# Optimization experiments

Hardware: AMD Instinct MI355X
Metric: run time of the kernel (lower is better)

## Reference

```python
import jax, jax.numpy as jnp
import numpy as np

B, S, D = 2, 2048, 768
H = 12
DH = D // H
EPS = 1e-12


def setup_inputs() -> dict:
    key = jax.random.key(0)
    ks = jax.random.split(key, 16)
    s = 0.02
    return {
        "hidden_states": jax.random.normal(ks[0], (B, S, D), jnp.float32),
        "attention_mask": jnp.zeros((B, 1, 1, S), jnp.float32),
        "position_bias": jax.random.normal(ks[1], (1, H, S, S), jnp.float32),
        "q_w": jax.random.normal(ks[2], (D, D), jnp.float32) * s,
        "q_b": jnp.zeros((D,), jnp.float32),
        "k_w": jax.random.normal(ks[3], (D, D), jnp.float32) * s,
        "k_b": jnp.zeros((D,), jnp.float32),
        "v_w": jax.random.normal(ks[4], (D, D), jnp.float32) * s,
        "v_b": jnp.zeros((D,), jnp.float32),
        "o_w": jax.random.normal(ks[5], (D, D), jnp.float32) * s,
        "o_b": jnp.zeros((D,), jnp.float32),
        "ln_w": jnp.ones((D,), jnp.float32),
        "ln_b": jnp.zeros((D,), jnp.float32),
    }


def _split_heads(x):
    # [B, S, D] -> [B, H, S, DH]
    b, s, _ = x.shape
    return x.reshape(b, s, H, DH).transpose(0, 2, 1, 3)


def reference(hidden_states, attention_mask, position_bias,
              q_w, q_b, k_w, k_b, v_w, v_b, o_w, o_b, ln_w, ln_b):
    # nn.Linear: y = x @ W.T + b (W stored [out, in])
    q = _split_heads(hidden_states @ q_w.T + q_b)
    k = _split_heads(hidden_states @ k_w.T + k_b)
    v = _split_heads(hidden_states @ v_w.T + v_b)

    scale = 1.0 / jnp.sqrt(jnp.asarray(DH, hidden_states.dtype))
    scores = jnp.einsum('bhqd,bhkd->bhqk', q, k) * scale
    scores = scores + position_bias + attention_mask
    probs = jax.nn.softmax(scores, axis=-1)

    c = jnp.einsum('bhqk,bhkd->bhqd', probs, v)
    c = c.transpose(0, 2, 1, 3).reshape(hidden_states.shape[0], -1, D)
    o = c @ o_w.T + o_b

    # residual + LayerNorm (dropout is identity at eval)
    x = o + hidden_states
    mu = jnp.mean(x, axis=-1, keepdims=True)
    var = jnp.mean(jnp.square(x - mu), axis=-1, keepdims=True)
    out = (x - mu) * jax.lax.rsqrt(var + EPS) * ln_w + ln_b
    return out
```

## Files before the change

### kernel.cpp

```cpp
#include <hip/hip_runtime.h>
#include <math.h>

typedef unsigned short u16;
typedef float f32x4 __attribute__((ext_vector_type(4)));
typedef __bf16 bf16x8 __attribute__((ext_vector_type(8)));

#define B_ 2
#define S_ 2048
#define D_ 768
#define H_ 12
#define DH_ 64

__device__ __forceinline__ u16 f2bf(float x) {
  union { float f; unsigned u; } v; v.f = x;
  unsigned r = v.u + 0x7fffu + ((v.u >> 16) & 1u);
  return (u16)(r >> 16);
}

__device__ __forceinline__ f32x4 zero4() { f32x4 z = {0.f, 0.f, 0.f, 0.f}; return z; }

__device__ __forceinline__ f32x4 mfma16(bf16x8 a, bf16x8 b, f32x4 c) {
  return __builtin_amdgcn_mfma_f32_16x16x32_bf16(a, b, c, 0, 0, 0);
}

__device__ __forceinline__ void gload_lds16(const void* g, void* l) {
  __builtin_amdgcn_global_load_lds((const __attribute__((address_space(1))) void*)g,
                                   (__attribute__((address_space(3))) void*)l, 16, 0, 0);
}

__global__ void cvt_kernel(const float* __restrict__ hid, const float* __restrict__ qw,
                           const float* __restrict__ kw, const float* __restrict__ vw,
                           const float* __restrict__ ow, u16* __restrict__ Hb,
                           u16* __restrict__ Wb) {
  const int NH = B_ * S_ * D_;
  const int NW = D_ * D_;
  const int T4 = (NH + 4 * NW) >> 2;
  int stride = gridDim.x * blockDim.x;
  for (int i = blockIdx.x * blockDim.x + threadIdx.x; i < T4; i += stride) {
    int e = i << 2;
    const float* src; u16* dst;
    if (e < NH) { src = hid + e; dst = Hb + e; }
    else {
      int o = e - NH;
      int m = o / NW, oo = o - m * NW;
      src = (m == 0 ? qw : m == 1 ? kw : m == 2 ? vw : ow) + oo;
      dst = Wb + o;
    }
    f32x4 v = *(const f32x4*)src;
    uint2 o2;
    o2.x = (unsigned)f2bf(v[0]) | ((unsigned)f2bf(v[1]) << 16);
    o2.y = (unsigned)f2bf(v[2]) | ((unsigned)f2bf(v[3]) << 16);
    *(uint2*)dst = o2;
  }
}

#define BM 128
#define BN 128
#define BK 64

__global__ __launch_bounds__(256) void gemm_kernel(
    const u16* __restrict__ A, const u16* __restrict__ W,
    const float* __restrict__ bq, const float* __restrict__ bk, const float* __restrict__ bv,
    u16* __restrict__ Qb, u16* __restrict__ Kb, u16* __restrict__ Vtmp,
    float* __restrict__ Of, const float* __restrict__ bO, int mode)
{
  __shared__ __align__(16) u16 As[BM * BK];
  __shared__ __align__(16) u16 Bs[BN * BK];
  int t = threadIdx.x;
  int lane = t & 63, w = t >> 6;
  int wr = w >> 1, wc = w & 1;
  int l15 = lane & 15, l4 = lane >> 4;
  int m0 = blockIdx.y * BM, n0 = blockIdx.x * BN;

  f32x4 acc[4][4];
#pragma unroll
  for (int i = 0; i < 4; ++i)
#pragma unroll
    for (int j = 0; j < 4; ++j) acc[i][j] = zero4();

  const int K = D_;
  for (int k0 = 0; k0 < K; k0 += BK) {
    __syncthreads();
#pragma unroll
    for (int p = 0; p < 4; ++p) {
      int seg = p * 4 + w;
      int bd = seg * 64 + lane;
      int row = bd >> 3;
      int slot = (bd & 7) ^ (row & 7);
      gload_lds16(A + (size_t)(m0 + row) * K + k0 + slot * 8, (char*)As + seg * 1024);
      gload_lds16(W + (size_t)(n0 + row) * K + k0 + slot * 8, (char*)Bs + seg * 1024);
    }
    __syncthreads();
#pragma unroll
    for (int kk = 0; kk < 2; ++kk) {
      bf16x8 af[4], bfr[4];
#pragma unroll
      for (int i = 0; i < 4; ++i) {
        int ra = wr * 64 + i * 16 + l15;
        af[i] = *(const bf16x8*)((const char*)As + ra * 128 +
                                 ((kk * 64 + (l4 << 4)) ^ ((ra & 7) << 4)));
        int rb = wc * 64 + i * 16 + l15;
        bfr[i] = *(const bf16x8*)((const char*)Bs + rb * 128 +
                                  ((kk * 64 + (l4 << 4)) ^ ((rb & 7) << 4)));
      }
#pragma unroll
      for (int i = 0; i < 4; ++i)
#pragma unroll
        for (int j = 0; j < 4; ++j)
          acc[i][j] = mfma16(af[i], bfr[j], acc[i][j]);
    }
  }

  if (mode == 0) {
    int mat = n0 / D_;
    int ncol0 = (n0 - mat * D_) + wc * 64;
    const float* bias = (mat == 0) ? bq : (mat == 1 ? bk : bv);
    u16* outp = (mat == 0) ? Qb : (mat == 1 ? Kb : Vtmp);
    float scale = (mat == 0) ? 0.125f : 1.0f;
    int h = ncol0 >> 6;
#pragma unroll
    for (int j = 0; j < 4; ++j) {
      int d = j * 16 + l15;
      float bvv = bias[ncol0 + d];
#pragma unroll
      for (int i = 0; i < 4; ++i) {
#pragma unroll
        for (int r = 0; r < 4; ++r) {
          int m = m0 + wr * 64 + i * 16 + (l4 << 2) + r;
          int bb = m >> 11, ss = m & 2047;
          float val = (acc[i][j][r] + bvv) * scale;
          outp[(((size_t)bb * H_ + h) * S_ + ss) * DH_ + d] = f2bf(val);
        }
      }
    }
  } else {
#pragma unroll
    for (int j = 0; j < 4; ++j) {
      int n = n0 + wc * 64 + j * 16 + l15;
      float bvv = bO[n];
#pragma unroll
      for (int i = 0; i < 4; ++i) {
#pragma unroll
        for (int r = 0; r < 4; ++r) {
          int m = m0 + wr * 64 + i * 16 + (l4 << 2) + r;
          Of[(size_t)m * D_ + n] = acc[i][j][r] + bvv;
        }
      }
    }
  }
}

__global__ __launch_bounds__(256) void vtrans_kernel(const u16* __restrict__ V,
                                                     u16* __restrict__ Vt) {
  __shared__ __align__(16) u16 tile[64 * 64];
  int t = threadIdx.x;
  int s0 = blockIdx.x * 64;
  int bh = blockIdx.y;
  const u16* src = V + ((size_t)bh * S_ + s0) * DH_;
#pragma unroll
  for (int p = 0; p < 2; ++p) {
    int bd = t + p * 256;
    int row = bd >> 3, slot = bd & 7;
    uint4 v = *(const uint4*)(src + row * 64 + slot * 8);
    *(uint4*)((char*)tile + row * 128 + ((slot ^ (row & 7)) << 4)) = v;
  }
  __syncthreads();
  int d = t >> 2, sc = (t & 3) * 16;
  u16* dst = Vt + ((size_t)bh * DH_ + d) * S_ + s0 + sc;
  int colB = d * 2;
#pragma unroll
  for (int half = 0; half < 2; ++half) {
    u16 tmp[8] __attribute__((aligned(16)));
#pragma unroll
    for (int j = 0; j < 8; ++j) {
      int s = sc + half * 8 + j;
      tmp[j] = *(const u16*)((const char*)tile + s * 128 +
                             (((colB >> 4) ^ (s & 7)) << 4) + (colB & 15));
    }
    *(uint4*)(dst + half * 8) = *(const uint4*)tmp;
  }
}

__global__ __launch_bounds__(256) void attn_kernel(
    const u16* __restrict__ Qb, const u16* __restrict__ Kb, const u16* __restrict__ Vt,
    const float* __restrict__ bias, const float* __restrict__ mask, u16* __restrict__ Cb)
{
  __shared__ __align__(16) u16 Ks[64 * 64];
  __shared__ __align__(16) u16 Vs[64 * 64];
  __shared__ __align__(16) u16 Ps[4][16][72];
  int t = threadIdx.x, lane = t & 63, w = t >> 6;
  int q0 = blockIdx.x * 64, h = blockIdx.y, b = blockIdx.z;
  size_t bh = (size_t)b * H_ + h;
  const u16* Qp = Qb + (bh * S_ + q0) * DH_;
  const u16* Kp = Kb + bh * S_ * DH_;
  const u16* Vp = Vt + bh * DH_ * S_;
  const float* biasp = bias + ((size_t)h * S_ + q0) * S_;
  const float* maskp = mask + (size_t)b * S_;
  int l15 = lane & 15, l4 = lane >> 4;

  bf16x8 qf0, qf1;
  {
    const u16* qrow = Qp + (w * 16 + l15) * DH_;
    qf0 = *(const bf16x8*)(qrow + l4 * 8);
    qf1 = *(const bf16x8*)(qrow + 32 + l4 * 8);
  }

  f32x4 oacc[4];
#pragma unroll
  for (int i = 0; i < 4; ++i) oacc[i] = zero4();
  float mrow[4] = {-INFINITY, -INFINITY, -INFINITY, -INFINITY};
  float lrow[4] = {0.f, 0.f, 0.f, 0.f};

  for (int k0 = 0; k0 < S_; k0 += 64) {
    __syncthreads();
#pragma unroll
    for (int p = 0; p < 2; ++p) {
      int seg = p * 4 + w;
      int bd = seg * 64 + lane;
      int row = bd >> 3;
      int slot = (bd & 7) ^ (row & 7);
      gload_lds16(Kp + (size_t)(k0 + row) * DH_ + slot * 8, (char*)Ks + seg * 1024);
      gload_lds16(Vp + (size_t)row * S_ + k0 + slot * 8, (char*)Vs + seg * 1024);
    }
    __syncthreads();

    f32x4 sf[4];
#pragma unroll
    for (int kf = 0; kf < 4; ++kf) {
      int row = kf * 16 + l15;
      bf16x8 kb0 = *(const bf16x8*)((const char*)Ks + row * 128 +
                                    ((l4 << 4) ^ ((row & 7) << 4)));
      bf16x8 kb1 = *(const bf16x8*)((const char*)Ks + row * 128 +
                                    ((64 + (l4 << 4)) ^ ((row & 7) << 4)));
      f32x4 s0 = zero4();
      s0 = mfma16(qf0, kb0, s0);
      s0 = mfma16(qf1, kb1, s0);
      sf[kf] = s0;
    }

    float mk[4];
#pragma unroll
    for (int kf = 0; kf < 4; ++kf) mk[kf] = maskp[k0 + kf * 16 + l15];
#pragma unroll
    for (int r = 0; r < 4; ++r) {
      const float* brow = biasp + (size_t)(w * 16 + (l4 << 2) + r) * S_ + k0 + l15;
#pragma unroll
      for (int kf = 0; kf < 4; ++kf) sf[kf][r] += brow[kf * 16] + mk[kf];
    }

#pragma unroll
    for (int r = 0; r < 4; ++r) {
      float mx = fmaxf(fmaxf(sf[0][r], sf[1][r]), fmaxf(sf[2][r], sf[3][r]));
#pragma unroll
      for (int o = 1; o < 16; o <<= 1) mx = fmaxf(mx, __shfl_xor(mx, o, 64));
      float mnew = fmaxf(mrow[r], mx);
      float alpha = __expf(mrow[r] - mnew);
      mrow[r] = mnew;
      float ls = 0.f;
#pragma unroll
      for (int kf = 0; kf < 4; ++kf) {
        float p = __expf(sf[kf][r] - mnew);
        sf[kf][r] = p;
        ls += p;
      }
#pragma unroll
      for (int o = 1; o < 16; o <<= 1) ls += __shfl_xor(ls, o, 64);
      lrow[r] = lrow[r] * alpha + ls;
#pragma unroll
      for (int df = 0; df < 4; ++df) oacc[df][r] *= alpha;
    }

#pragma unroll
    for (int r = 0; r < 4; ++r)
#pragma unroll
      for (int kf = 0; kf < 4; ++kf)
        Ps[w][(l4 << 2) + r][kf * 16 + l15] = f2bf(sf[kf][r]);

    bf16x8 pa0 = *(const bf16x8*)&Ps[w][l15][l4 * 8];
    bf16x8 pa1 = *(const bf16x8*)&Ps[w][l15][32 + l4 * 8];

#pragma unroll
    for (int df = 0; df < 4; ++df) {
      int row = df * 16 + l15;
      bf16x8 vb0 = *(const bf16x8*)((const char*)Vs + row * 128 +
                                    ((l4 << 4) ^ ((row & 7) << 4)));
      bf16x8 vb1 = *(const bf16x8*)((const char*)Vs + row * 128 +
                                    ((64 + (l4 << 4)) ^ ((row & 7) << 4)));
      oacc[df] = mfma16(pa0, vb0, oacc[df]);
      oacc[df] = mfma16(pa1, vb1, oacc[df]);
    }
  }

#pragma unroll
  for (int r = 0; r < 4; ++r) {
    float inv = 1.0f / lrow[r];
    int q = q0 + w * 16 + (l4 << 2) + r;
    size_t base = ((size_t)b * S_ + q) * D_ + h * DH_ + l15;
#pragma unroll
    for (int df = 0; df < 4; ++df)
      Cb[base + df * 16] = f2bf(oacc[df][r] * inv);
  }
}

__global__ __launch_bounds__(192) void ln_kernel(const float* __restrict__ O,
                                                 const float* __restrict__ hid,
                                                 const float* __restrict__ lw,
                                                 const float* __restrict__ lb,
                                                 float* __restrict__ out) {
  int row = blockIdx.x, t = threadIdx.x;
  size_t base = (size_t)row * D_;
  f32x4 x = *(const f32x4*)(O + base + t * 4);
  f32x4 hh = *(const f32x4*)(hid + base + t * 4);
  x = x + hh;
  float s = x[0] + x[1] + x[2] + x[3];
  float s2 = x[0] * x[0] + x[1] * x[1] + x[2] * x[2] + x[3] * x[3];
#pragma unroll
  for (int o = 1; o < 64; o <<= 1) {
    s += __shfl_xor(s, o, 64);
    s2 += __shfl_xor(s2, o, 64);
  }
  __shared__ float rs[3], rs2[3];
  int w = t >> 6, lane = t & 63;
  if (lane == 0) { rs[w] = s; rs2[w] = s2; }
  __syncthreads();
  s = rs[0] + rs[1] + rs[2];
  s2 = rs2[0] + rs2[1] + rs2[2];
  float mu = s * (1.0f / 768.0f);
  float var = s2 * (1.0f / 768.0f) - mu * mu;
  float rstd = rsqrtf(var + 1e-12f);
  f32x4 w4 = *(const f32x4*)(lw + t * 4);
  f32x4 b4 = *(const f32x4*)(lb + t * 4);
  f32x4 y = (x - mu) * rstd * w4 + b4;
  *(f32x4*)(out + base + t * 4) = y;
}

extern "C" void kernel_launch(void* const* d_in, const int* in_sizes, int n_in,
                              void* d_out, int out_size, void* d_ws, size_t ws_size,
                              hipStream_t stream) {
  const float* hid  = (const float*)d_in[0];
  const float* mask = (const float*)d_in[1];
  const float* bias = (const float*)d_in[2];
  const float* qw = (const float*)d_in[3];
  const float* qb = (const float*)d_in[4];
  const float* kw = (const float*)d_in[5];
  const float* kb = (const float*)d_in[6];
  const float* vw = (const float*)d_in[7];
  const float* vb = (const float*)d_in[8];
  const float* ow = (const float*)d_in[9];
  const float* ob = (const float*)d_in[10];
  const float* lnw = (const float*)d_in[11];
  const float* lnb = (const float*)d_in[12];

  char* ws = (char*)d_ws;
  const size_t NHB = (size_t)B_ * S_ * D_ * 2;
  const size_t NWB = (size_t)4 * D_ * D_ * 2;
  const size_t NQB = (size_t)B_ * H_ * S_ * DH_ * 2;
  u16* Hb = (u16*)ws;
  u16* Wb = (u16*)(ws + NHB);
  u16* Qb = (u16*)(ws + NHB + NWB);
  u16* Kb = (u16*)(ws + NHB + NWB + NQB);
  u16* Vt = (u16*)(ws + NHB + NWB + 2 * NQB);
  u16* Cb = (u16*)(ws + NHB + NWB + 3 * NQB);
  float* Of = (float*)(ws + NHB + NWB + 4 * NQB);
  u16* Vtmp = (u16*)Of;

  cvt_kernel<<<2048, 256, 0, stream>>>(hid, qw, kw, vw, ow, Hb, Wb);

  gemm_kernel<<<dim3(18, 32), 256, 0, stream>>>(
      Hb, Wb, qb, kb, vb, Qb, Kb, Vtmp, nullptr, nullptr, 0);

  vtrans_kernel<<<dim3(S_ / 64, B_ * H_), 256, 0, stream>>>(Vtmp, Vt);

  attn_kernel<<<dim3(S_ / 64, H_, B_), 256, 0, stream>>>(Qb, Kb, Vt, bias, mask, Cb);

  gemm_kernel<<<dim3(6, 32), 256, 0, stream>>>(
      Cb, Wb + (size_t)3 * D_ * D_, nullptr, nullptr, nullptr,
      nullptr, nullptr, nullptr, Of, ob, 1);

  ln_kernel<<<B_ * S_, 192, 0, stream>>>(Of, hid, lnw, lnb, (float*)d_out);
}
```

Baseline: 177.3 us.

## Double-buffer K/V tiles and prefetch position bias into registers

Double-buffers the K and V shared-memory tiles so the next tile's global-to-LDS loads are issued before computing on the current tile. The next tile's position-bias values are prefetched into registers, and the mask row is staged once into shared memory. This is meant to hide global load latency, especially for the large fp32 bias stream, behind the MFMA and softmax work. In exchange it doubles K/V LDS use and adds an 8 KB mask buffer plus extra registers, which may lower occupancy. The barrier at the loop end only works if gload_lds completion is ordered by __syncthreads.

```diff
diff --git a/kernel.cpp b/kernel.cpp
--- a/kernel.cpp
+++ b/kernel.cpp
@@ -185,9 +185,10 @@
     const u16* __restrict__ Qb, const u16* __restrict__ Kb, const u16* __restrict__ Vt,
     const float* __restrict__ bias, const float* __restrict__ mask, u16* __restrict__ Cb)
 {
-  __shared__ __align__(16) u16 Ks[64 * 64];
-  __shared__ __align__(16) u16 Vs[64 * 64];
+  __shared__ __align__(16) u16 Ks[2][64 * 64];
+  __shared__ __align__(16) u16 Vs[2][64 * 64];
   __shared__ __align__(16) u16 Ps[4][16][72];
+  __shared__ __align__(16) float Ms[S_];
   int t = threadIdx.x, lane = t & 63, w = t >> 6;
   int q0 = blockIdx.x * 64, h = blockIdx.y, b = blockIdx.z;
   size_t bh = (size_t)b * H_ + h;
@@ -198,6 +199,11 @@
   const float* maskp = mask + (size_t)b * S_;
   int l15 = lane & 15, l4 = lane >> 4;
 
+  const float* brp0 = biasp + (size_t)(w * 16 + (l4 << 2) + 0) * S_ + l15;
+  const float* brp1 = brp0 + S_;
+  const float* brp2 = brp1 + S_;
+  const float* brp3 = brp2 + S_;
+
   bf16x8 qf0, qf1;
   {
     const u16* qrow = Qp + (w * 16 + l15) * DH_;
@@ -211,26 +217,66 @@
   float mrow[4] = {-INFINITY, -INFINITY, -INFINITY, -INFINITY};
   float lrow[4] = {0.f, 0.f, 0.f, 0.f};
 
-  for (int k0 = 0; k0 < S_; k0 += 64) {
-    __syncthreads();
-#pragma unroll
-    for (int p = 0; p < 2; ++p) {
-      int seg = p * 4 + w;
-      int bd = seg * 64 + lane;
-      int row = bd >> 3;
-      int slot = (bd & 7) ^ (row & 7);
-      gload_lds16(Kp + (size_t)(k0 + row) * DH_ + slot * 8, (char*)Ks + seg * 1024);
-      gload_lds16(Vp + (size_t)row * S_ + k0 + slot * 8, (char*)Vs + seg * 1024);
-    }
-    __syncthreads();
+  float bc0[4], bc1[4], bc2[4], bc3[4];
+  float bn0[4], bn1[4], bn2[4], bn3[4];
+
+#pragma unroll
+  for (int p = 0; p < 2; ++p) {
+    int seg = p * 4 + w;
+    int bd = seg * 64 + lane;
+    int row = bd >> 3;
+    int slot = (bd & 7) ^ (row & 7);
+    gload_lds16(Kp + (size_t)row * DH_ + slot * 8, (char*)Ks[0] + seg * 1024);
+    gload_lds16(Vp + (size_t)row * S_ + slot * 8, (char*)Vs[0] + seg * 1024);
+  }
+#pragma unroll
+  for (int p = 0; p < 2; ++p) {
+    int seg = p * 4 + w;
+    gload_lds16(maskp + seg * 256 + lane * 4, (char*)Ms + seg * 1024);
+  }
+#pragma unroll
+  for (int kf = 0; kf < 4; ++kf) {
+    bc0[kf] = brp0[kf * 16];
+    bc1[kf] = brp1[kf * 16];
+    bc2[kf] = brp2[kf * 16];
+    bc3[kf] = brp3[kf * 16];
+  }
+  __syncthreads();
+
+  int cur = 0;
+  for (int kt = 0; kt < S_ / 64; ++kt) {
+    int k0 = kt * 64;
+    if (kt + 1 < S_ / 64) {
+      int k0n = k0 + 64;
+      const u16* Kn = Kp + (size_t)k0n * DH_;
+#pragma unroll
+      for (int p = 0; p < 2; ++p) {
+        int seg = p * 4 + w;
+        int bd = seg * 64 + lane;
+        int row = bd >> 3;
+        int slot = (bd & 7) ^ (row & 7);
+        gload_lds16(Kn + (size_t)row * DH_ + slot * 8, (char*)Ks[cur ^ 1] + seg * 1024);
+        gload_lds16(Vp + (size_t)row * S_ + k0n + slot * 8, (char*)Vs[cur ^ 1] + seg * 1024);
+      }
+#pragma unroll
+      for (int kf = 0; kf < 4; ++kf) {
+        bn0[kf] = brp0[k0n + kf * 16];
+        bn1[kf] = brp1[k0n + kf * 16];
+        bn2[kf] = brp2[k0n + kf * 16];
+        bn3[kf] = brp3[k0n + kf * 16];
+      }
+    }
+
+    const u16* Kc = Ks[cur];
+    const u16* Vc = Vs[cur];
 
     f32x4 sf[4];
 #pragma unroll
     for (int kf = 0; kf < 4; ++kf) {
       int row = kf * 16 + l15;
-      bf16x8 kb0 = *(const bf16x8*)((const char*)Ks + row * 128 +
+      bf16x8 kb0 = *(const bf16x8*)((const char*)Kc + row * 128 +
                                     ((l4 << 4) ^ ((row & 7) << 4)));
-      bf16x8 kb1 = *(const bf16x8*)((const char*)Ks + row * 128 +
+      bf16x8 kb1 = *(const bf16x8*)((const char*)Kc + row * 128 +
                                     ((64 + (l4 << 4)) ^ ((row & 7) << 4)));
       f32x4 s0 = zero4();
       s0 = mfma16(qf0, kb0, s0);
@@ -238,14 +284,13 @@
       sf[kf] = s0;
     }
 
-    float mk[4];
-#pragma unroll
-    for (int kf = 0; kf < 4; ++kf) mk[kf] = maskp[k0 + kf * 16 + l15];
-#pragma unroll
-    for (int r = 0; r < 4; ++r) {
-      const float* brow = biasp + (size_t)(w * 16 + (l4 << 2) + r) * S_ + k0 + l15;
-#pragma unroll
-      for (int kf = 0; kf < 4; ++kf) sf[kf][r] += brow[kf * 16] + mk[kf];
+#pragma unroll
+    for (int kf = 0; kf < 4; ++kf) {
+      float mk = Ms[k0 + kf * 16 + l15];
+      sf[kf][0] += bc0[kf] + mk;
+      sf[kf][1] += bc1[kf] + mk;
+      sf[kf][2] += bc2[kf] + mk;
+      sf[kf][3] += bc3[kf] + mk;
     }
 
 #pragma unroll
@@ -282,12 +327,20 @@
 #pragma unroll
     for (int df = 0; df < 4; ++df) {
       int row = df * 16 + l15;
-      bf16x8 vb0 = *(const bf16x8*)((const char*)Vs + row * 128 +
+      bf16x8 vb0 = *(const bf16x8*)((const char*)Vc + row * 128 +
                                     ((l4 << 4) ^ ((row & 7) << 4)));
-      bf16x8 vb1 = *(const bf16x8*)((const char*)Vs + row * 128 +
+      bf16x8 vb1 = *(const bf16x8*)((const char*)Vc + row * 128 +
                                     ((64 + (l4 << 4)) ^ ((row & 7) << 4)));
       oacc[df] = mfma16(pa0, vb0, oacc[df]);
       oacc[df] = mfma16(pa1, vb1, oacc[df]);
+    }
+
+    __syncthreads();
+    cur ^= 1;
+#pragma unroll
+    for (int kf = 0; kf < 4; ++kf) {
+      bc0[kf] = bn0[kf]; bc1[kf] = bn1[kf];
+      bc2[kf] = bn2[kf]; bc3[kf] = bn3[kf];
     }
   }
 
```

Result: faster. 173.4 us (-2.2%).
